# Kernel tuning notes

Measured on AMD Instinct MI355X. Metric: run time of the kernel, lower is better.

## Reference

```python
import jax, jax.numpy as jnp
import numpy as np
import math

HIDDEN = 256
NUM_HEADS = 8
HEAD_DIM = HIDDEN // NUM_HEADS  # 32
SCALE = math.sqrt(HEAD_DIM)
B, N, E = 1, 20000, 320000


def setup_inputs() -> dict:
    key = jax.random.key(0)
    kq, kk, kv, ke = jax.random.split(key, 4)
    q = jax.random.normal(kq, (B, N, HIDDEN), dtype=jnp.float32)
    k = jax.random.normal(kk, (B, N, HIDDEN), dtype=jnp.float32)
    v = jax.random.normal(kv, (B, N, HIDDEN), dtype=jnp.float32)
    edge_index = jax.random.randint(ke, (2, E), 0, N, dtype=jnp.int64)
    return {"q": q, "k": k, "v": v, "edge_index": edge_index}


def reference(q, k, v, edge_index):
    batch_size, node_num = q.shape[0], q.shape[1]
    # flatten batch*node axis, split heads: [B*N, H, D]
    qf = q.reshape(-1, NUM_HEADS, HEAD_DIM)
    kf = k.reshape(-1, NUM_HEADS, HEAD_DIM)
    vf = v.reshape(-1, NUM_HEADS, HEAD_DIM)
    src_idx = edge_index[0]
    dst_idx = edge_index[1]
    src = kf[src_idx]    # [E, H, D] gathered keys
    dest = qf[dst_idx]   # [E, H, D] gathered queries
    # unnormalized exp score per edge/head, clamped like the torch code
    score = jnp.clip(jnp.sum(src * dest, axis=-1, keepdims=True) / SCALE, -5.0, 5.0)
    score = jnp.exp(score)                 # [E, H, 1]
    msg = vf[src_idx] * score              # [E, H, D]
    num_seg = qf.shape[0]
    wV = jax.ops.segment_sum(msg, dst_idx, num_segments=num_seg)    # [B*N, H, D]
    Z = jax.ops.segment_sum(score, dst_idx, num_segments=num_seg)   # [B*N, H, 1]
    x = wV / (Z + 1e-6)
    return x.reshape(batch_size, node_num, -1)
```

## Files before the change

kernel.cpp:

```cpp
#include <hip/hip_runtime.h>
#include <hip/hip_fp16.h>
#include <math.h>

#define NHEADS 8
#define HIDDEN 256
#define F4_PER_ROW 64
#define INV_SCALE 0.17677669529663687f
#define ELL_W 64

#define SCAN_THREADS 1024
#define SCAN_CHUNK 20


union H4 { float2 f; __half2 h[2]; };
union KV8 { float4 f4; __half2 h2[4]; };

__global__ void __launch_bounds__(256)
build_kernel(const float4* __restrict__ kf4, const float4* __restrict__ vf4,
             char* __restrict__ kvh,
             const int* __restrict__ src, const int* __restrict__ dst,
             int* __restrict__ cnt, int* __restrict__ ell,
             int nf4, int N, int E) {
    int stride = gridDim.x * blockDim.x;
    int tid0 = blockIdx.x * blockDim.x + threadIdx.x;

    for (int i = tid0; i < nf4; i += stride) {
        int n = i >> 6;
        int c = i & 63;
        int hk = c >> 3;
        int off = (c & 7) * 8;
        char* bb = kvh + ((size_t)hk * N + n) * 128 + off;
        float4 x = kf4[i];
        H4 u;
        u.h[0] = __floats2half2_rn(x.x, x.y);
        u.h[1] = __floats2half2_rn(x.z, x.w);
        *(float2*)bb = u.f;
        float4 y = vf4[i];
        H4 w;
        w.h[0] = __floats2half2_rn(y.x, y.y);
        w.h[1] = __floats2half2_rn(y.z, y.w);
        *(float2*)(bb + 64) = w.f;
    }

    int nq = E >> 2;
    for (int q = tid0; q < nq; q += stride) {
        int4 s = ((const int4*)src)[q];
        int4 d = ((const int4*)dst)[q];
        int sl;
        sl = atomicAdd(&cnt[d.x], 1); if (sl < ELL_W) ell[d.x * ELL_W + sl] = s.x;
        sl = atomicAdd(&cnt[d.y], 1); if (sl < ELL_W) ell[d.y * ELL_W + sl] = s.y;
        sl = atomicAdd(&cnt[d.z], 1); if (sl < ELL_W) ell[d.z * ELL_W + sl] = s.z;
        sl = atomicAdd(&cnt[d.w], 1); if (sl < ELL_W) ell[d.w * ELL_W + sl] = s.w;
    }
    if (tid0 == 0) {
        for (int i = (E >> 2) << 2; i < E; ++i) {
            int t = dst[i];
            int sl = atomicAdd(&cnt[t], 1);
            if (sl < ELL_W) ell[t * ELL_W + sl] = src[i];
        }
    }
}

__global__ void __launch_bounds__(256)
gather_hs_kernel(const float* __restrict__ qf, const char* __restrict__ kvh,
                 const int* __restrict__ cnt, const int* __restrict__ ell,
                 float* __restrict__ outf, int N) {
    int b = blockIdx.x;
    int h = b & 7;
    int wid = threadIdx.x >> 6;
    int lane = threadIdx.x & 63;
    int t = (b >> 3) * 4 + wid;
    if (t >= N) return;

    int sub = lane & 7;
    int eg  = lane >> 3;

    const float* qsl = qf + (size_t)t * HIDDEN + h * 32;
    float* ob = outf + (size_t)t * HIDDEN + h * 32;

    int deg = cnt[t];
    deg = deg < ELL_W ? deg : ELL_W;

    if (deg == 0) {
        if (eg == 0 && sub >= 4) {
            float4 zr = make_float4(0.f, 0.f, 0.f, 0.f);
            ((float4*)ob)[(sub - 4) * 2]     = zr;
            ((float4*)ob)[(sub - 4) * 2 + 1] = zr;
        }
        return;
    }

    const int* lst = ell + (size_t)t * ELL_W;
    int idxreg = 0;
    if (lane < deg) idxreg = lst[lane];

    int qsub = sub & 3;
    float4 qa = ((const float4*)qsl)[qsub * 2];
    float4 qb = ((const float4*)qsl)[qsub * 2 + 1];

    const char* base = kvh + (size_t)h * N * 128;

    float acc[8] = {0.f, 0.f, 0.f, 0.f, 0.f, 0.f, 0.f, 0.f};
    float z = 0.f;

    int nb = (deg + 7) >> 3;
    for (int it = 0; it < nb; ++it) {
        int p = it * 8 + eg;
        int pc = p < deg ? p : deg - 1;
        int s = __shfl(idxreg, pc, 64);
        KV8 u;
        u.f4 = *(const float4*)(base + (size_t)s * 128 + sub * 16);

        float2 a0 = __half22float2(u.h2[0]);
        float2 a1 = __half22float2(u.h2[1]);
        float2 a2 = __half22float2(u.h2[2]);
        float2 a3 = __half22float2(u.h2[3]);
        float r = a0.x * qa.x + a0.y * qa.y + a1.x * qa.z + a1.y * qa.w
                + a2.x * qb.x + a2.y * qb.y + a3.x * qb.z + a3.y * qb.w;
        r += __shfl_xor(r, 1, 8);
        r += __shfl_xor(r, 2, 8);
        float sc = __expf(fminf(fmaxf(r * INV_SCALE, -5.f), 5.f));
        sc = __shfl(sc, lane & ~7, 64);
        sc = (p < deg) ? sc : 0.f;
        z += sc;
        acc[0] += a0.x * sc; acc[1] += a0.y * sc;
        acc[2] += a1.x * sc; acc[3] += a1.y * sc;
        acc[4] += a2.x * sc; acc[5] += a2.y * sc;
        acc[6] += a3.x * sc; acc[7] += a3.y * sc;
    }

    #pragma unroll
    for (int m = 8; m < 64; m <<= 1) {
        z += __shfl_xor(z, m, 64);
        #pragma unroll
        for (int d = 0; d < 8; ++d) acc[d] += __shfl_xor(acc[d], m, 64);
    }

    float inv = 1.f / (z + 1e-6f);
    if (eg == 0 && sub >= 4) {
        int j = sub - 4;
        float4 o1 = make_float4(acc[0] * inv, acc[1] * inv, acc[2] * inv, acc[3] * inv);
        float4 o2 = make_float4(acc[4] * inv, acc[5] * inv, acc[6] * inv, acc[7] * inv);
        ((float4*)ob)[j * 2]     = o1;
        ((float4*)ob)[j * 2 + 1] = o2;
    }
}


__global__ void __launch_bounds__(256)
histogram_kernel(const int* __restrict__ dst, int* __restrict__ cnt, int E) {
    int i = (blockIdx.x * blockDim.x + threadIdx.x) * 4;
    if (i + 3 < E) {
        int4 d = *(const int4*)(dst + i);
        atomicAdd(&cnt[d.x], 1);
        atomicAdd(&cnt[d.y], 1);
        atomicAdd(&cnt[d.z], 1);
        atomicAdd(&cnt[d.w], 1);
    } else {
        for (; i < E; ++i) atomicAdd(&cnt[dst[i]], 1);
    }
}

__global__ void __launch_bounds__(SCAN_THREADS)
scan_kernel(const int* __restrict__ cnt, int* __restrict__ off, int N) {
    __shared__ int wsum[16];
    __shared__ int wpre[16];
    int t = threadIdx.x;
    int lane = t & 63;
    int wv = t >> 6;
    int base = t * SCAN_CHUNK;
    int local[SCAN_CHUNK];
    int sum = 0;
    #pragma unroll
    for (int j = 0; j < SCAN_CHUNK; ++j) {
        int i = base + j;
        int c = (i < N) ? cnt[i] : 0;
        local[j] = c;
        sum += c;
    }
    int x = sum;
    #pragma unroll
    for (int d = 1; d < 64; d <<= 1) {
        int y = __shfl_up(x, d, 64);
        if (lane >= d) x += y;
    }
    if (lane == 63) wsum[wv] = x;
    __syncthreads();
    if (t < 16) {
        int v = wsum[t];
        #pragma unroll
        for (int d = 1; d < 16; d <<= 1) {
            int y = __shfl_up(v, d, 16);
            if (t >= d) v += y;
        }
        wpre[t] = v;
    }
    __syncthreads();
    int run = (wv ? wpre[wv - 1] : 0) + (x - sum);
    #pragma unroll
    for (int j = 0; j < SCAN_CHUNK; ++j) {
        int i = base + j;
        if (i <= N) off[i] = run;
        run += local[j];
    }
}

__global__ void __launch_bounds__(256)
scatter_kernel(const int* __restrict__ src, const int* __restrict__ dst,
               const int* __restrict__ off, int* __restrict__ cnt,
               int* __restrict__ csr_src, int E) {
    int i = (blockIdx.x * blockDim.x + threadIdx.x) * 4;
    if (i + 3 < E) {
        int4 s = *(const int4*)(src + i);
        int4 d = *(const int4*)(dst + i);
        csr_src[off[d.x] + atomicSub(&cnt[d.x], 1) - 1] = s.x;
        csr_src[off[d.y] + atomicSub(&cnt[d.y], 1) - 1] = s.y;
        csr_src[off[d.z] + atomicSub(&cnt[d.z], 1) - 1] = s.z;
        csr_src[off[d.w] + atomicSub(&cnt[d.w], 1) - 1] = s.w;
    } else {
        for (; i < E; ++i) {
            int t = dst[i];
            csr_src[off[t] + atomicSub(&cnt[t], 1) - 1] = src[i];
        }
    }
}

__device__ __forceinline__ float dot4(float4 a, float4 b) {
    return a.x * b.x + a.y * b.y + a.z * b.z + a.w * b.w;
}

__device__ __forceinline__ float hred8(float p) {
    #pragma unroll
    for (int m = 1; m < 8; m <<= 1) p += __shfl_xor(p, m, 8);
    return p;
}

__global__ void __launch_bounds__(256)
gather_kernel(const float4* __restrict__ q4, const float4* __restrict__ k4,
              const float4* __restrict__ v4, const int* __restrict__ csr_src,
              const int* __restrict__ off, float4* __restrict__ out4, int N) {
    int wid  = threadIdx.x >> 6;
    int lane = threadIdx.x & 63;
    int t = blockIdx.x * 4 + wid;
    if (t >= N) return;

    int beg = off[t], end = off[t + 1];
    long trow = (long)t * F4_PER_ROW;
    float4 qv = q4[trow + lane];

    float4 acc = make_float4(0.f, 0.f, 0.f, 0.f);
    float z = 0.f;

    for (int i = beg; i < end; ++i) {
        int s = csr_src[i];
        long r = (long)s * F4_PER_ROW + lane;
        float4 kv = k4[r];
        float4 vv = v4[r];
        float p = hred8(dot4(kv, qv));
        float sc = __expf(fminf(fmaxf(p * INV_SCALE, -5.f), 5.f));
        acc.x += vv.x * sc;
        acc.y += vv.y * sc;
        acc.z += vv.z * sc;
        acc.w += vv.w * sc;
        z += sc;
    }

    float inv = 1.f / (z + 1e-6f);
    float4 o;
    o.x = acc.x * inv; o.y = acc.y * inv; o.z = acc.z * inv; o.w = acc.w * inv;
    out4[trow + lane] = o;
}


extern "C" void kernel_launch(void* const* d_in, const int* in_sizes, int n_in,
                              void* d_out, int out_size, void* d_ws, size_t ws_size,
                              hipStream_t stream) {
    const float* qf = (const float*)d_in[0];
    const float* kf = (const float*)d_in[1];
    const float* vf = (const float*)d_in[2];
    const int*   ei = (const int*)d_in[3];

    int E = in_sizes[3] / 2;
    int N = in_sizes[0] / HIDDEN;
    int nf4 = in_sizes[0] / 4;

    const int* src = ei;
    const int* dst = ei + E;

    size_t need = (size_t)N * 1024 + (size_t)N * ELL_W * 4 + (size_t)N * 4 + 256;

    if (ws_size >= need) {
        char* p = (char*)d_ws;
        char* kvh = p;                       p += (size_t)N * 1024;
        int*  ell = (int*)p;                 p += (size_t)N * ELL_W * 4;
        int*  cnt = (int*)p;

        hipMemsetAsync(cnt, 0, (size_t)N * sizeof(int), stream);
        build_kernel<<<4096, 256, 0, stream>>>(
            (const float4*)kf, (const float4*)vf, kvh,
            src, dst, cnt, ell, nf4, N, E);
        int ngrp = (N + 3) / 4;
        gather_hs_kernel<<<8 * ngrp, 256, 0, stream>>>(
            qf, kvh, cnt, ell, (float*)d_out, N);
    } else {
        int* cnt = (int*)d_ws;
        int* off = cnt + N;
        int* csr = off + N + 1;

        hipMemsetAsync(cnt, 0, (size_t)N * sizeof(int), stream);
        int eb = (E / 4 + 255) / 256 + 1;
        histogram_kernel<<<eb, 256, 0, stream>>>(dst, cnt, E);
        scan_kernel<<<1, SCAN_THREADS, 0, stream>>>(cnt, off, N);
        scatter_kernel<<<eb, 256, 0, stream>>>(src, dst, off, cnt, csr, E);
        gather_kernel<<<(N + 3) / 4, 256, 0, stream>>>(
            (const float4*)qf, (const float4*)kf, (const float4*)vf,
            csr, off, (float4*)d_out, N);
    }
}
```

Measured before the change: 184.1 us.

## Interleave fp16 K/V per lane and gather with 16-lane DPP reductions

The build kernel now packs K and V halves interleaved so each lane reads one float2 holding a K pair and the matching V pair. The gather kernel assigns 16 lanes per (node, head) instead of a full wave, so one wave covers four nodes. It walks edges sequentially, using DPP row reductions in place of shuffles, and exp2 with a pre-scaled clamp. This cuts shuffle and reduction overhead and lane waste on low-degree nodes, but each load is now small (8 bytes per lane) and edges are processed serially, which may expose gather latency.

New measurement: 192.8 us. +4.7%, slower.

```diff
diff --git a/kernel.cpp b/kernel.cpp
--- a/kernel.cpp
+++ b/kernel.cpp
@@ -6,40 +6,43 @@
 #define HIDDEN 256
 #define F4_PER_ROW 64
 #define INV_SCALE 0.17677669529663687f
+#define C2 0.2550352f
+#define CLAMP2 7.2134752f
 #define ELL_W 64
 
 #define SCAN_THREADS 1024
 #define SCAN_CHUNK 20
 
-
-union H4 { float2 f; __half2 h[2]; };
-union KV8 { float4 f4; __half2 h2[4]; };
 
 __global__ void __launch_bounds__(256)
 build_kernel(const float4* __restrict__ kf4, const float4* __restrict__ vf4,
              char* __restrict__ kvh,
              const int* __restrict__ src, const int* __restrict__ dst,
              int* __restrict__ cnt, int* __restrict__ ell,
-             int nf4, int N, int E) {
+             int N, int E) {
     int stride = gridDim.x * blockDim.x;
     int tid0 = blockIdx.x * blockDim.x + threadIdx.x;
 
-    for (int i = tid0; i < nf4; i += stride) {
-        int n = i >> 6;
-        int c = i & 63;
-        int hk = c >> 3;
-        int off = (c & 7) * 8;
-        char* bb = kvh + ((size_t)hk * N + n) * 128 + off;
-        float4 x = kf4[i];
-        H4 u;
-        u.h[0] = __floats2half2_rn(x.x, x.y);
-        u.h[1] = __floats2half2_rn(x.z, x.w);
-        *(float2*)bb = u.f;
-        float4 y = vf4[i];
-        H4 w;
-        w.h[0] = __floats2half2_rn(y.x, y.y);
-        w.h[1] = __floats2half2_rn(y.z, y.w);
-        *(float2*)(bb + 64) = w.f;
+    int nconv = N * NHEADS;
+    for (int i = tid0; i < nconv; i += stride) {
+        int n = i >> 3;
+        int h = i & 7;
+        const float4* kb = kf4 + (size_t)n * 64 + h * 8;
+        const float4* vb = vf4 + (size_t)n * 64 + h * 8;
+        float4* row = (float4*)(kvh + ((size_t)h * N + n) * 128);
+        #pragma unroll
+        for (int j = 0; j < 8; ++j) {
+            float4 kx = kb[j];
+            float4 vx = vb[j];
+            __half2 a = __floats2half2_rn(kx.x, kx.y);
+            __half2 b = __floats2half2_rn(vx.x, vx.y);
+            __half2 c = __floats2half2_rn(kx.z, kx.w);
+            __half2 d = __floats2half2_rn(vx.z, vx.w);
+            float4 o;
+            o.x = *(float*)&a; o.y = *(float*)&b;
+            o.z = *(float*)&c; o.w = *(float*)&d;
+            row[j] = o;
+        }
     }
 
     int nq = E >> 2;
@@ -61,89 +64,60 @@
     }
 }
 
-__global__ void __launch_bounds__(256)
-gather_hs_kernel(const float* __restrict__ qf, const char* __restrict__ kvh,
-                 const int* __restrict__ cnt, const int* __restrict__ ell,
-                 float* __restrict__ outf, int N) {
+__device__ __forceinline__ float row_reduce16(float x) {
+    union FI { float f; int i; };
+    FI a; a.f = x;
+    FI b;
+    b.i = __builtin_amdgcn_update_dpp(0, a.i, 0x128, 0xF, 0xF, false); a.f += b.f;
+    b.i = __builtin_amdgcn_update_dpp(0, a.i, 0x124, 0xF, 0xF, false); a.f += b.f;
+    b.i = __builtin_amdgcn_update_dpp(0, a.i, 0x122, 0xF, 0xF, false); a.f += b.f;
+    b.i = __builtin_amdgcn_update_dpp(0, a.i, 0x121, 0xF, 0xF, false); a.f += b.f;
+    return a.f;
+}
+
+__global__ void __launch_bounds__(256)
+gather_dpp_kernel(const float* __restrict__ qf, const char* __restrict__ kvh,
+                  const int* __restrict__ cnt, const int* __restrict__ ell,
+                  float* __restrict__ outf, int N) {
     int b = blockIdx.x;
     int h = b & 7;
-    int wid = threadIdx.x >> 6;
+    int wave = threadIdx.x >> 6;
     int lane = threadIdx.x & 63;
-    int t = (b >> 3) * 4 + wid;
+    int g = lane >> 4;
+    int sub = lane & 15;
+    int t = (b >> 3) * 16 + wave * 4 + g;
     if (t >= N) return;
-
-    int sub = lane & 7;
-    int eg  = lane >> 3;
-
-    const float* qsl = qf + (size_t)t * HIDDEN + h * 32;
-    float* ob = outf + (size_t)t * HIDDEN + h * 32;
 
     int deg = cnt[t];
     deg = deg < ELL_W ? deg : ELL_W;
-
-    if (deg == 0) {
-        if (eg == 0 && sub >= 4) {
-            float4 zr = make_float4(0.f, 0.f, 0.f, 0.f);
-            ((float4*)ob)[(sub - 4) * 2]     = zr;
-            ((float4*)ob)[(sub - 4) * 2 + 1] = zr;
-        }
-        return;
-    }
-
     const int* lst = ell + (size_t)t * ELL_W;
-    int idxreg = 0;
-    if (lane < deg) idxreg = lst[lane];
-
-    int qsub = sub & 3;
-    float4 qa = ((const float4*)qsl)[qsub * 2];
-    float4 qb = ((const float4*)qsl)[qsub * 2 + 1];
-
-    const char* base = kvh + (size_t)h * N * 128;
-
-    float acc[8] = {0.f, 0.f, 0.f, 0.f, 0.f, 0.f, 0.f, 0.f};
-    float z = 0.f;
-
-    int nb = (deg + 7) >> 3;
-    for (int it = 0; it < nb; ++it) {
-        int p = it * 8 + eg;
-        int pc = p < deg ? p : deg - 1;
-        int s = __shfl(idxreg, pc, 64);
-        KV8 u;
-        u.f4 = *(const float4*)(base + (size_t)s * 128 + sub * 16);
-
-        float2 a0 = __half22float2(u.h2[0]);
-        float2 a1 = __half22float2(u.h2[1]);
-        float2 a2 = __half22float2(u.h2[2]);
-        float2 a3 = __half22float2(u.h2[3]);
-        float r = a0.x * qa.x + a0.y * qa.y + a1.x * qa.z + a1.y * qa.w
-                + a2.x * qb.x + a2.y * qb.y + a3.x * qb.z + a3.y * qb.w;
-        r += __shfl_xor(r, 1, 8);
-        r += __shfl_xor(r, 2, 8);
-        float sc = __expf(fminf(fmaxf(r * INV_SCALE, -5.f), 5.f));
-        sc = __shfl(sc, lane & ~7, 64);
-        sc = (p < deg) ? sc : 0.f;
+
+    const float* qp = qf + (size_t)t * HIDDEN + h * 32 + 2 * sub;
+    float q0 = qp[0], q1 = qp[1];
+
+    const char* base = kvh + (size_t)h * N * 128 + (size_t)sub * 8;
+
+    float acc0 = 0.f, acc1 = 0.f, z = 0.f;
+
+    for (int i = 0; i < deg; ++i) {
+        int s = lst[i];
+        float2 rw = *(const float2*)(base + (size_t)s * 128);
+        __half2 kh = *(__half2*)&rw.x;
+        __half2 vh = *(__half2*)&rw.y;
+        float2 kf2 = __half22float2(kh);
+        float r = kf2.x * q0 + kf2.y * q1;
+        r = row_reduce16(r);
+        float sc = exp2f(fminf(fmaxf(r * C2, -CLAMP2), CLAMP2));
         z += sc;
-        acc[0] += a0.x * sc; acc[1] += a0.y * sc;
-        acc[2] += a1.x * sc; acc[3] += a1.y * sc;
-        acc[4] += a2.x * sc; acc[5] += a2.y * sc;
-        acc[6] += a3.x * sc; acc[7] += a3.y * sc;
-    }
-
-    #pragma unroll
-    for (int m = 8; m < 64; m <<= 1) {
-        z += __shfl_xor(z, m, 64);
-        #pragma unroll
-        for (int d = 0; d < 8; ++d) acc[d] += __shfl_xor(acc[d], m, 64);
+        float2 vf2 = __half22float2(vh);
+        acc0 += vf2.x * sc;
+        acc1 += vf2.y * sc;
     }
 
     float inv = 1.f / (z + 1e-6f);
-    if (eg == 0 && sub >= 4) {
-        int j = sub - 4;
-        float4 o1 = make_float4(acc[0] * inv, acc[1] * inv, acc[2] * inv, acc[3] * inv);
-        float4 o2 = make_float4(acc[4] * inv, acc[5] * inv, acc[6] * inv, acc[7] * inv);
-        ((float4*)ob)[j * 2]     = o1;
-        ((float4*)ob)[j * 2 + 1] = o2;
-    }
+    float* op = outf + (size_t)t * HIDDEN + h * 32 + 2 * sub;
+    op[0] = acc0 * inv;
+    op[1] = acc1 * inv;
 }
 
 
@@ -282,7 +256,6 @@
 
     int E = in_sizes[3] / 2;
     int N = in_sizes[0] / HIDDEN;
-    int nf4 = in_sizes[0] / 4;
 
     const int* src = ei;
     const int* dst = ei + E;
@@ -296,11 +269,11 @@
         int*  cnt = (int*)p;
 
         hipMemsetAsync(cnt, 0, (size_t)N * sizeof(int), stream);
-        build_kernel<<<4096, 256, 0, stream>>>(
+        build_kernel<<<2048, 256, 0, stream>>>(
             (const float4*)kf, (const float4*)vf, kvh,
-            src, dst, cnt, ell, nf4, N, E);
-        int ngrp = (N + 3) / 4;
-        gather_hs_kernel<<<8 * ngrp, 256, 0, stream>>>(
+            src, dst, cnt, ell, N, E);
+        int ngrp = (N + 15) / 16;
+        gather_dpp_kernel<<<8 * ngrp, 256, 0, stream>>>(
             qf, kvh, cnt, ell, (float*)d_out, N);
     } else {
         int* cnt = (int*)d_ws;
```
